# Kernel optimization log

Measured on AMD Instinct MI355X. Metric: run time of the kernel, lower is better.

Reference implementation:

```python
import jax, jax.numpy as jnp
import numpy as np

B, P, EPG = 1000, 100, 1200  # graphs, nodes/graph, edges/graph
IN, HID, OUT, K = 16, 64, 5, 3


def setup_inputs() -> dict:
    key = jax.random.key(0)
    ks = jax.random.split(key, 12)
    offs = jnp.repeat(jnp.arange(B, dtype=jnp.int32) * P, EPG)
    src = jax.random.randint(ks[0], (B * EPG,), 0, P, dtype=jnp.int32) + offs
    dst = jax.random.randint(ks[1], (B * EPG,), 0, P, dtype=jnp.int32) + offs
    graph_ids = jnp.repeat(jnp.arange(B, dtype=jnp.int32), P)
    feat = jax.random.normal(ks[2], (B * P, IN), dtype=jnp.float32)

    def lin(k1, fan_in, fan_out):
        s = 1.0 / np.sqrt(fan_in)
        return jax.random.uniform(k1, (fan_in, fan_out), jnp.float32, -s, s)

    return {
        'feat': feat, 'src': src, 'dst': dst, 'graph_ids': graph_ids,
        'n_graphs': B,
        'W1': lin(ks[3], K * IN, HID), 'b1': jnp.zeros((HID,), jnp.float32),
        'W2': lin(ks[4], K * HID, HID), 'b2': jnp.zeros((HID,), jnp.float32),
        'W3': lin(ks[5], K * HID, HID), 'b3': jnp.zeros((HID,), jnp.float32),
        'Wfc': lin(ks[6], HID, OUT), 'bfc': jnp.zeros((OUT,), jnp.float32),
    }


def _cheb_conv(x, src, dst, d_invsqrt, W, b, k):
    # DGL ChebConv with lambda_max=2 -> re_norm=1, scaled Laplacian = -D^-1/2 A D^-1/2
    n = x.shape[0]

    def Ax(h):
        msg = (h * d_invsqrt)[src]                      # gather from source nodes
        agg = jax.ops.segment_sum(msg, dst, num_segments=n)
        return agg * d_invsqrt

    Xs = [x]
    if k > 1:
        Xs.append(-Ax(Xs[0]))                           # X1 = L_hat X0
        for _ in range(2, k):
            Xs.append(-2.0 * Ax(Xs[-1]) - Xs[-2])       # X_i = 2 L_hat X_{i-1} - X_{i-2}
    Xt = jnp.concatenate(Xs, axis=1)                    # [n, k*f]
    return Xt @ W + b


def reference(feat, src, dst, graph_ids, n_graphs, W1, b1, W2, b2, W3, b3, Wfc, bfc):
    n = feat.shape[0]
    deg = jax.ops.segment_sum(jnp.ones((src.shape[0],), feat.dtype), dst, num_segments=n)
    d_invsqrt = jnp.where(deg < 1.0, 1.0, deg) ** -0.5
    d_invsqrt = d_invsqrt[:, None]

    h = jax.nn.relu(_cheb_conv(feat, src, dst, d_invsqrt, W1, b1, K))
    h = jax.nn.relu(_cheb_conv(h, src, dst, d_invsqrt, W2, b2, K))
    h = jax.nn.relu(_cheb_conv(h, src, dst, d_invsqrt, W3, b3, K))

    # dgl.mean_nodes: per-graph mean pooling
    counts = jax.ops.segment_sum(jnp.ones((n,), h.dtype), graph_ids, num_segments=n_graphs)
    hg = jax.ops.segment_sum(h, graph_ids, num_segments=n_graphs) / counts[:, None]
    return hg @ Wfc + bfc
```

## Files before the change

### kernel.cpp

```cpp
#include <hip/hip_runtime.h>

#define NGRAPH 1000
#define P      100
#define EPG    1200
#define INF    16
#define HID    64
#define NOUT   5


#define ASTR   100
#define T1OFF  64
#define T2OFF  80

#define AINT_K  128
#define AINT_SZ (P * AINT_K)

#define RK1 64
#define RK2 208
#define L1HI 0
#define L1LO 4096
#define L2HI 8192
#define L2LO 21504
#define L3HI 34816
#define L3LO 48128
#define WT_SHORTS 61440

typedef short short8 __attribute__((ext_vector_type(8)));
typedef float f32x4  __attribute__((ext_vector_type(4)));
typedef int   int4v  __attribute__((ext_vector_type(4)));

__device__ __forceinline__ int sw(int row, int col) {
    return row * ASTR + (col ^ (((row >> 3) & 3) << 3));
}

__device__ __forceinline__ unsigned packsplit(float x) {
    unsigned u  = __float_as_uint(x);
    unsigned hi = (u + 0x7fffu + ((u >> 16) & 1u)) >> 16;
    float r = x - __uint_as_float(hi << 16);
    unsigned v  = __float_as_uint(r);
    unsigned lo = (v + 0x7fffu + ((v >> 16) & 1u)) >> 16;
    return (hi << 16) | (lo & 0xffffu);
}

__device__ __forceinline__ float unpack(unsigned p) {
    return __uint_as_float(p & 0xffff0000u) + __uint_as_float(p << 16);
}

#define PSEL_HI 0x07060302u
#define PSEL_LO 0x05040100u

__global__ __launch_bounds__(256) void wprep(
    const float* __restrict__ W1, const float* __restrict__ W2,
    const float* __restrict__ W3, short* __restrict__ wt)
{
    const int i0 = blockIdx.x * blockDim.x + threadIdx.x;
    const int stride = gridDim.x * blockDim.x;
    for (int e = i0; e < HID * RK1; e += stride) {
        int c = e / RK1, r = e % RK1;
        float v = (r < 3 * INF) ? W1[r * HID + c] : 0.f;
        unsigned p = packsplit(v);
        wt[L1HI + e] = (short)(p >> 16);
        wt[L1LO + e] = (short)(p & 0xffffu);
    }
    for (int e = i0; e < HID * RK2; e += stride) {
        int c = e / RK2, r = e % RK2;
        float v2 = (r < 3 * HID) ? W2[r * HID + c] : 0.f;
        float v3 = (r < 3 * HID) ? W3[r * HID + c] : 0.f;
        unsigned p2 = packsplit(v2), p3 = packsplit(v3);
        wt[L2HI + e] = (short)(p2 >> 16); wt[L2LO + e] = (short)(p2 & 0xffffu);
        wt[L3HI + e] = (short)(p3 >> 16); wt[L3LO + e] = (short)(p3 & 0xffffu);
    }
}

__global__ __launch_bounds__(256) void abuild(
    const int* __restrict__ src, const int* __restrict__ dst,
    short* __restrict__ aint)
{
    __shared__ unsigned int cnt[AINT_SZ / 2];
    const int g = blockIdx.x, tid = threadIdx.x, base = g * P;
    for (int i = tid; i < AINT_SZ / 2; i += 256) cnt[i] = 0u;
    __syncthreads();
    const int* srcg = src + g * EPG;
    const int* dstg = dst + g * EPG;
    for (int e = tid; e < EPG; e += 256) {
        int s = srcg[e] - base;
        int d = dstg[e] - base;
        int idx = d * AINT_K + s;
        atomicAdd(&cnt[idx >> 1], 1u << ((idx & 1) * 16));
    }
    __syncthreads();
    unsigned int* outw = (unsigned int*)(aint + (size_t)g * AINT_SZ);
    for (int i = tid; i < AINT_SZ / 2; i += 256) {
        unsigned int u = cnt[i];
        unsigned int b0 = __float_as_uint((float)(u & 0xffffu)) >> 16;
        unsigned int b1 = __float_as_uint((float)(u >> 16)) >> 16;
        outw[i] = b0 | (b1 << 16);
    }
}

template <int SECOND>
__device__ __forceinline__ void dense_prop(
    unsigned* __restrict__ Ap,
    short8 a00, short8 a01, short8 a02, short8 a03,
    short8 a10, short8 a11, short8 a12, short8 a13,
    bool has2, int srcoff, int dstoff, int ycb,
    int rb0, int rb1, f32x4 dv0, f32x4 dv1, int lane)
{
    const int n16 = lane & 15;
    const int q   = lane >> 4;
    const int kq  = q * 8;
    const int c   = srcoff + n16;
    f32x4 p0, p1;
    p0[0]=0.f; p0[1]=0.f; p0[2]=0.f; p0[3]=0.f;
    p1[0]=0.f; p1[1]=0.f; p1[2]=0.f; p1[3]=0.f;

#define PROPK(KK, A0, A1) { \
    const int rr = KK * 32 + kq; \
    const unsigned u0 = Ap[sw((KK < 3 || rr + 0 < P) ? rr + 0 : 0, c)]; \
    const unsigned u1 = Ap[sw((KK < 3 || rr + 1 < P) ? rr + 1 : 0, c)]; \
    const unsigned u2 = Ap[sw((KK < 3 || rr + 2 < P) ? rr + 2 : 0, c)]; \
    const unsigned u3 = Ap[sw((KK < 3 || rr + 3 < P) ? rr + 3 : 0, c)]; \
    const unsigned u4 = Ap[sw((KK < 3 || rr + 4 < P) ? rr + 4 : 0, c)]; \
    const unsigned u5 = Ap[sw((KK < 3 || rr + 5 < P) ? rr + 5 : 0, c)]; \
    const unsigned u6 = Ap[sw((KK < 3 || rr + 6 < P) ? rr + 6 : 0, c)]; \
    const unsigned u7 = Ap[sw((KK < 3 || rr + 7 < P) ? rr + 7 : 0, c)]; \
    int4v hh, ll; \
    hh[0] = (int)__builtin_amdgcn_perm(u1, u0, PSEL_HI); \
    hh[1] = (int)__builtin_amdgcn_perm(u3, u2, PSEL_HI); \
    hh[2] = (int)__builtin_amdgcn_perm(u5, u4, PSEL_HI); \
    hh[3] = (int)__builtin_amdgcn_perm(u7, u6, PSEL_HI); \
    ll[0] = (int)__builtin_amdgcn_perm(u1, u0, PSEL_LO); \
    ll[1] = (int)__builtin_amdgcn_perm(u3, u2, PSEL_LO); \
    ll[2] = (int)__builtin_amdgcn_perm(u5, u4, PSEL_LO); \
    ll[3] = (int)__builtin_amdgcn_perm(u7, u6, PSEL_LO); \
    const short8 bhi = __builtin_bit_cast(short8, hh); \
    const short8 blo = __builtin_bit_cast(short8, ll); \
    p0 = __builtin_amdgcn_mfma_f32_16x16x32_bf16(A0, bhi, p0, 0, 0, 0); \
    p0 = __builtin_amdgcn_mfma_f32_16x16x32_bf16(A0, blo, p0, 0, 0, 0); \
    if (has2) { \
        p1 = __builtin_amdgcn_mfma_f32_16x16x32_bf16(A1, bhi, p1, 0, 0, 0); \
        p1 = __builtin_amdgcn_mfma_f32_16x16x32_bf16(A1, blo, p1, 0, 0, 0); \
    } }

    PROPK(0, a00, a10)
    PROPK(1, a01, a11)
    PROPK(2, a02, a12)
    PROPK(3, a03, a13)
#undef PROPK

#pragma unroll
    for (int r = 0; r < 4; r++) {
        const int row = rb0 + q * 4 + r;
        const float d2 = dv0[r] * dv0[r];
        float o;
        if (SECOND) o = -2.f * d2 * p0[r] - unpack(Ap[sw(row, ycb + n16)]);
        else        o = -d2 * p0[r];
        Ap[sw(row, dstoff + n16)] = packsplit(o);
    }
    if (has2) {
#pragma unroll
        for (int r = 0; r < 4; r++) {
            const int row = rb1 + q * 4 + r;
            if (rb1 != 84 || row >= 96) {
                const float d2 = dv1[r] * dv1[r];
                float o;
                if (SECOND) o = -2.f * d2 * p1[r] - unpack(Ap[sw(row, ycb + n16)]);
                else        o = -d2 * p1[r];
                Ap[sw(row, dstoff + n16)] = packsplit(o);
            }
        }
    }
}

template <int F, int FINAL>
__device__ __forceinline__ void cheb_layer(
    unsigned* __restrict__ Ap, const float* __restrict__ dinv,
    short8 a00, short8 a01, short8 a02, short8 a03,
    short8 a10, short8 a11, short8 a12, short8 a13, bool has2,
    const short* __restrict__ whi, const short* __restrict__ wlo,
    const float* __restrict__ bias,
    int tid, int rb0, int rb1, f32x4 dv0, f32x4 dv1)
{
    const int RK   = 3 * F + 16;
    const int lane = tid & 63;
    const int wv   = tid >> 6;
    const int n16  = lane & 15;
    const int q    = lane >> 4;
    const int ncol = (wv << 4) + n16;

    f32x4 acc[7];
#pragma unroll
    for (int t = 0; t < 7; t++) { acc[t][0]=0.f; acc[t][1]=0.f; acc[t][2]=0.f; acc[t][3]=0.f; }

    for (int cb = 0; cb < F; cb += 16) {
        dense_prop<0>(Ap, a00,a01,a02,a03, a10,a11,a12,a13, has2,
                      cb,    T1OFF, 0,  rb0, rb1, dv0, dv1, lane);
        __syncthreads();
        dense_prop<1>(Ap, a00,a01,a02,a03, a10,a11,a12,a13, has2,
                      T1OFF, T2OFF, cb, rb0, rb1, dv0, dv1, lane);
        __syncthreads();

#pragma unroll
        for (int ks = 0; ks < 2; ks++) {
            int wr, aoff;
            if (ks == 0) {
                wr   = (q == 0) ? cb : (q == 1) ? cb + 8 : (q == 2) ? F + cb : F + cb + 8;
                aoff = (q == 0) ? cb : (q == 1) ? cb + 8 : (q == 2) ? T1OFF  : T1OFF + 8;
            } else {
                wr   = (q == 0) ? 2*F + cb : (q == 1) ? 2*F + cb + 8 : (q == 2) ? 3*F : 3*F + 8;
                aoff = (q == 0) ? T2OFF    : (q == 1) ? T2OFF + 8    : (q == 2) ? T1OFF : T1OFF + 8;
            }
            const short8 bhi = *(const short8*)&whi[ncol * RK + wr];
            const short8 blo = *(const short8*)&wlo[ncol * RK + wr];
#pragma unroll
            for (int t = 0; t < 7; t++) {
                const int row = ((t < 6) ? t * 16 : 84) + n16;
                const unsigned* xp = &Ap[sw(row, aoff)];
                const int4v w0 = *(const int4v*)xp;
                const int4v w1 = *(const int4v*)(xp + 4);
                int4v hh, ll;
                hh[0] = (int)__builtin_amdgcn_perm((unsigned)w0[1], (unsigned)w0[0], PSEL_HI);
                hh[1] = (int)__builtin_amdgcn_perm((unsigned)w0[3], (unsigned)w0[2], PSEL_HI);
                hh[2] = (int)__builtin_amdgcn_perm((unsigned)w1[1], (unsigned)w1[0], PSEL_HI);
                hh[3] = (int)__builtin_amdgcn_perm((unsigned)w1[3], (unsigned)w1[2], PSEL_HI);
                ll[0] = (int)__builtin_amdgcn_perm((unsigned)w0[1], (unsigned)w0[0], PSEL_LO);
                ll[1] = (int)__builtin_amdgcn_perm((unsigned)w0[3], (unsigned)w0[2], PSEL_LO);
                ll[2] = (int)__builtin_amdgcn_perm((unsigned)w1[1], (unsigned)w1[0], PSEL_LO);
                ll[3] = (int)__builtin_amdgcn_perm((unsigned)w1[3], (unsigned)w1[2], PSEL_LO);
                const short8 ahi = __builtin_bit_cast(short8, hh);
                const short8 alo = __builtin_bit_cast(short8, ll);
                acc[t] = __builtin_amdgcn_mfma_f32_16x16x32_bf16(ahi, bhi, acc[t], 0, 0, 0);
                acc[t] = __builtin_amdgcn_mfma_f32_16x16x32_bf16(ahi, blo, acc[t], 0, 0, 0);
                acc[t] = __builtin_amdgcn_mfma_f32_16x16x32_bf16(alo, bhi, acc[t], 0, 0, 0);
            }
        }
        __syncthreads();
    }

    const float bcol = bias[ncol];
#pragma unroll
    for (int t = 0; t < 7; t++) {
        const int rbase = ((t < 6) ? t * 16 : 84) + q * 4;
#pragma unroll
        for (int r = 0; r < 4; r++) {
            const int row = rbase + r;
            if (t < 6 || row >= 96) {
                const float dn = dinv[row];
                const float v = acc[t][r];
                float o;
                if (FINAL) o = fmaxf(v * (1.0f / dn) + bcol, 0.f);
                else       o = fmaxf(v + bcol * dn, 0.f);
                Ap[sw(row, ncol)] = packsplit(o);
            }
        }
    }
    __syncthreads();
}

__global__ __launch_bounds__(256, 4) void gnn_kernel(
    const float* __restrict__ feat,
    const int* __restrict__ src, const int* __restrict__ dst,
    const float* __restrict__ b1, const float* __restrict__ b2,
    const float* __restrict__ b3,
    const float* __restrict__ Wfc, const float* __restrict__ bfc,
    const short* __restrict__ wt, const short* __restrict__ aint,
    float* __restrict__ out)
{
    __shared__ __align__(16) unsigned Ap[P * ASTR];
    __shared__ float meta[128];

    const int g = blockIdx.x;
    const int tid = threadIdx.x;
    const int base = g * P;
    const int* dstg = dst + g * EPG;

    int* deg = (int*)meta;
    for (int i = tid; i < P; i += 256) deg[i] = 0;
    __syncthreads();
    for (int e = tid; e < EPG; e += 256) atomicAdd(&deg[dstg[e] - base], 1);
    __syncthreads();
    for (int i = tid; i < P; i += 256) {
        int dg = deg[i];
        meta[i] = rsqrtf((float)(dg > 1 ? dg : 1));
    }
    __syncthreads();

    for (int i = tid; i < P * INF / 4; i += 256) {
        int n = i >> 2, f0 = (i & 3) * 4;
        float4 v = *(const float4*)&feat[(size_t)base * INF + i * 4];
        float dn = meta[n];
        int4v pk;
        pk[0] = (int)packsplit(v.x * dn);
        pk[1] = (int)packsplit(v.y * dn);
        pk[2] = (int)packsplit(v.z * dn);
        pk[3] = (int)packsplit(v.w * dn);
        *(int4v*)&Ap[sw(n, f0)] = pk;
    }
    __syncthreads();

    const int lane = tid & 63, wv = tid >> 6, q = lane >> 4, n16 = lane & 15;
    const int rb0 = wv * 16;
    const int t2i = wv + 4;
    const int rb1 = (t2i >= 6) ? 84 : t2i * 16;
    const bool has2 = (wv < 3);
    f32x4 dv0, dv1;
#pragma unroll
    for (int r = 0; r < 4; r++) {
        dv0[r] = meta[rb0 + q * 4 + r];
        dv1[r] = meta[(has2 ? rb1 : rb0) + q * 4 + r];
    }
    const short* aintg = aint + (size_t)g * AINT_SZ;
    const int arow0 = rb0 + n16;
    const int arow1 = (has2 ? rb1 : rb0) + n16;
    const short8 a00 = *(const short8*)&aintg[arow0 * AINT_K +  0 + q * 8];
    const short8 a01 = *(const short8*)&aintg[arow0 * AINT_K + 32 + q * 8];
    const short8 a02 = *(const short8*)&aintg[arow0 * AINT_K + 64 + q * 8];
    const short8 a03 = *(const short8*)&aintg[arow0 * AINT_K + 96 + q * 8];
    const short8 a10 = *(const short8*)&aintg[arow1 * AINT_K +  0 + q * 8];
    const short8 a11 = *(const short8*)&aintg[arow1 * AINT_K + 32 + q * 8];
    const short8 a12 = *(const short8*)&aintg[arow1 * AINT_K + 64 + q * 8];
    const short8 a13 = *(const short8*)&aintg[arow1 * AINT_K + 96 + q * 8];

    cheb_layer<INF, 0>(Ap, meta, a00,a01,a02,a03, a10,a11,a12,a13, has2,
                       wt + L1HI, wt + L1LO, b1, tid, rb0, rb1, dv0, dv1);
    cheb_layer<HID, 0>(Ap, meta, a00,a01,a02,a03, a10,a11,a12,a13, has2,
                       wt + L2HI, wt + L2LO, b2, tid, rb0, rb1, dv0, dv1);
    cheb_layer<HID, 1>(Ap, meta, a00,a01,a02,a03, a10,a11,a12,a13, has2,
                       wt + L3HI, wt + L3LO, b3, tid, rb0, rb1, dv0, dv1);

    {
        const int l = tid & 63, w = tid >> 6;
        float s = 0.f;
        for (int n = w; n < P; n += 4) s += unpack(Ap[sw(n, l)]);
        float o0 = s * Wfc[l * NOUT + 0];
        float o1 = s * Wfc[l * NOUT + 1];
        float o2 = s * Wfc[l * NOUT + 2];
        float o3 = s * Wfc[l * NOUT + 3];
        float o4 = s * Wfc[l * NOUT + 4];
#pragma unroll
        for (int d = 1; d < 64; d <<= 1) {
            o0 += __shfl_xor(o0, d);
            o1 += __shfl_xor(o1, d);
            o2 += __shfl_xor(o2, d);
            o3 += __shfl_xor(o3, d);
            o4 += __shfl_xor(o4, d);
        }
        if (l == 0) {
            meta[100 + w * NOUT + 0] = o0;
            meta[100 + w * NOUT + 1] = o1;
            meta[100 + w * NOUT + 2] = o2;
            meta[100 + w * NOUT + 3] = o3;
            meta[100 + w * NOUT + 4] = o4;
        }
    }
    __syncthreads();
    if (tid < NOUT) {
        float o = meta[100 + tid] + meta[105 + tid] + meta[110 + tid] + meta[115 + tid];
        out[g * NOUT + tid] = bfc[tid] + o * (1.0f / P);
    }
}

extern "C" void kernel_launch(void* const* d_in, const int* in_sizes, int n_in,
                              void* d_out, int out_size, void* d_ws, size_t ws_size,
                              hipStream_t stream)
{
    const float* feat = (const float*)d_in[0];
    const int*   src  = (const int*)d_in[1];
    const int*   dst  = (const int*)d_in[2];
    const float* W1  = (const float*)d_in[5];
    const float* b1  = (const float*)d_in[6];
    const float* W2  = (const float*)d_in[7];
    const float* b2  = (const float*)d_in[8];
    const float* W3  = (const float*)d_in[9];
    const float* b3  = (const float*)d_in[10];
    const float* Wfc = (const float*)d_in[11];
    const float* bfc = (const float*)d_in[12];
    float* out = (float*)d_out;

    short* wt   = (short*)d_ws;
    short* aint = wt + WT_SHORTS;

    wprep<<<64, 256, 0, stream>>>(W1, W2, W3, wt);
    abuild<<<NGRAPH, 256, 0, stream>>>(src, dst, aint);
    gnn_kernel<<<NGRAPH, 256, 0, stream>>>(feat, src, dst,
                                           b1, b2, b3, Wfc, bfc, wt, aint, out);
}
```

Before: 180.8 us.

## Fuse adjacency build into main kernel and split feature LDS into hi/lo planes

```diff
diff --git a/kernel.cpp b/kernel.cpp
--- a/kernel.cpp
+++ b/kernel.cpp
@@ -8,12 +8,9 @@
 #define NOUT   5
 
 
-#define ASTR   100
+#define FSTR   96
 #define T1OFF  64
 #define T2OFF  80
-
-#define AINT_K  128
-#define AINT_SZ (P * AINT_K)
 
 #define RK1 64
 #define RK2 208
@@ -23,14 +20,12 @@
 #define L2LO 21504
 #define L3HI 34816
 #define L3LO 48128
-#define WT_SHORTS 61440
 
 typedef short short8 __attribute__((ext_vector_type(8)));
 typedef float f32x4  __attribute__((ext_vector_type(4)));
-typedef int   int4v  __attribute__((ext_vector_type(4)));
-
-__device__ __forceinline__ int sw(int row, int col) {
-    return row * ASTR + (col ^ (((row >> 3) & 3) << 3));
+
+__device__ __forceinline__ int swf(int row, int col) {
+    return row * FSTR + (col ^ (((row >> 3) & 3) << 3));
 }
 
 __device__ __forceinline__ unsigned packsplit(float x) {
@@ -42,12 +37,10 @@
     return (hi << 16) | (lo & 0xffffu);
 }
 
-__device__ __forceinline__ float unpack(unsigned p) {
-    return __uint_as_float(p & 0xffff0000u) + __uint_as_float(p << 16);
-}
-
-#define PSEL_HI 0x07060302u
-#define PSEL_LO 0x05040100u
+__device__ __forceinline__ float up2(short h, short l) {
+    return __uint_as_float(((unsigned)(unsigned short)h) << 16) +
+           __uint_as_float(((unsigned)(unsigned short)l) << 16);
+}
 
 __global__ __launch_bounds__(256) void wprep(
     const float* __restrict__ W1, const float* __restrict__ W2,
@@ -72,35 +65,9 @@
     }
 }
 
-__global__ __launch_bounds__(256) void abuild(
-    const int* __restrict__ src, const int* __restrict__ dst,
-    short* __restrict__ aint)
-{
-    __shared__ unsigned int cnt[AINT_SZ / 2];
-    const int g = blockIdx.x, tid = threadIdx.x, base = g * P;
-    for (int i = tid; i < AINT_SZ / 2; i += 256) cnt[i] = 0u;
-    __syncthreads();
-    const int* srcg = src + g * EPG;
-    const int* dstg = dst + g * EPG;
-    for (int e = tid; e < EPG; e += 256) {
-        int s = srcg[e] - base;
-        int d = dstg[e] - base;
-        int idx = d * AINT_K + s;
-        atomicAdd(&cnt[idx >> 1], 1u << ((idx & 1) * 16));
-    }
-    __syncthreads();
-    unsigned int* outw = (unsigned int*)(aint + (size_t)g * AINT_SZ);
-    for (int i = tid; i < AINT_SZ / 2; i += 256) {
-        unsigned int u = cnt[i];
-        unsigned int b0 = __float_as_uint((float)(u & 0xffffu)) >> 16;
-        unsigned int b1 = __float_as_uint((float)(u >> 16)) >> 16;
-        outw[i] = b0 | (b1 << 16);
-    }
-}
-
 template <int SECOND>
 __device__ __forceinline__ void dense_prop(
-    unsigned* __restrict__ Ap,
+    short* __restrict__ Ahi, short* __restrict__ Alo,
     short8 a00, short8 a01, short8 a02, short8 a03,
     short8 a10, short8 a11, short8 a12, short8 a13,
     bool has2, int srcoff, int dstoff, int ycb,
@@ -109,32 +76,38 @@
     const int n16 = lane & 15;
     const int q   = lane >> 4;
     const int kq  = q * 8;
-    const int c   = srcoff + n16;
+    const int c = (srcoff + n16) ^ (q << 3);
     f32x4 p0, p1;
     p0[0]=0.f; p0[1]=0.f; p0[2]=0.f; p0[3]=0.f;
     p1[0]=0.f; p1[1]=0.f; p1[2]=0.f; p1[3]=0.f;
 
 #define PROPK(KK, A0, A1) { \
-    const int rr = KK * 32 + kq; \
-    const unsigned u0 = Ap[sw((KK < 3 || rr + 0 < P) ? rr + 0 : 0, c)]; \
-    const unsigned u1 = Ap[sw((KK < 3 || rr + 1 < P) ? rr + 1 : 0, c)]; \
-    const unsigned u2 = Ap[sw((KK < 3 || rr + 2 < P) ? rr + 2 : 0, c)]; \
-    const unsigned u3 = Ap[sw((KK < 3 || rr + 3 < P) ? rr + 3 : 0, c)]; \
-    const unsigned u4 = Ap[sw((KK < 3 || rr + 4 < P) ? rr + 4 : 0, c)]; \
-    const unsigned u5 = Ap[sw((KK < 3 || rr + 5 < P) ? rr + 5 : 0, c)]; \
-    const unsigned u6 = Ap[sw((KK < 3 || rr + 6 < P) ? rr + 6 : 0, c)]; \
-    const unsigned u7 = Ap[sw((KK < 3 || rr + 7 < P) ? rr + 7 : 0, c)]; \
-    int4v hh, ll; \
-    hh[0] = (int)__builtin_amdgcn_perm(u1, u0, PSEL_HI); \
-    hh[1] = (int)__builtin_amdgcn_perm(u3, u2, PSEL_HI); \
-    hh[2] = (int)__builtin_amdgcn_perm(u5, u4, PSEL_HI); \
-    hh[3] = (int)__builtin_amdgcn_perm(u7, u6, PSEL_HI); \
-    ll[0] = (int)__builtin_amdgcn_perm(u1, u0, PSEL_LO); \
-    ll[1] = (int)__builtin_amdgcn_perm(u3, u2, PSEL_LO); \
-    ll[2] = (int)__builtin_amdgcn_perm(u5, u4, PSEL_LO); \
-    ll[3] = (int)__builtin_amdgcn_perm(u7, u6, PSEL_LO); \
-    const short8 bhi = __builtin_bit_cast(short8, hh); \
-    const short8 blo = __builtin_bit_cast(short8, ll); \
+    const int b0 = (KK * 32 + kq) * FSTR + c; \
+    short8 bhi, blo; \
+    if (KK < 3) { \
+        bhi[0]=Ahi[b0        ]; blo[0]=Alo[b0        ]; \
+        bhi[1]=Ahi[b0+1*FSTR ]; blo[1]=Alo[b0+1*FSTR ]; \
+        bhi[2]=Ahi[b0+2*FSTR ]; blo[2]=Alo[b0+2*FSTR ]; \
+        bhi[3]=Ahi[b0+3*FSTR ]; blo[3]=Alo[b0+3*FSTR ]; \
+        bhi[4]=Ahi[b0+4*FSTR ]; blo[4]=Alo[b0+4*FSTR ]; \
+        bhi[5]=Ahi[b0+5*FSTR ]; blo[5]=Alo[b0+5*FSTR ]; \
+        bhi[6]=Ahi[b0+6*FSTR ]; blo[6]=Alo[b0+6*FSTR ]; \
+        bhi[7]=Ahi[b0+7*FSTR ]; blo[7]=Alo[b0+7*FSTR ]; \
+    } else { \
+        const int m0 = 96 + kq; \
+        const int i0 = (m0+0 < P ? (m0+0)*FSTR : 0) + c; \
+        const int i1 = (m0+1 < P ? (m0+1)*FSTR : 0) + c; \
+        const int i2 = (m0+2 < P ? (m0+2)*FSTR : 0) + c; \
+        const int i3 = (m0+3 < P ? (m0+3)*FSTR : 0) + c; \
+        bhi[0]=Ahi[i0]; blo[0]=Alo[i0]; \
+        bhi[1]=Ahi[i1]; blo[1]=Alo[i1]; \
+        bhi[2]=Ahi[i2]; blo[2]=Alo[i2]; \
+        bhi[3]=Ahi[i3]; blo[3]=Alo[i3]; \
+        bhi[4]=0; blo[4]=0; \
+        bhi[5]=0; blo[5]=0; \
+        bhi[6]=0; blo[6]=0; \
+        bhi[7]=0; blo[7]=0; \
+    } \
     p0 = __builtin_amdgcn_mfma_f32_16x16x32_bf16(A0, bhi, p0, 0, 0, 0); \
     p0 = __builtin_amdgcn_mfma_f32_16x16x32_bf16(A0, blo, p0, 0, 0, 0); \
     if (has2) { \
@@ -153,9 +126,13 @@
         const int row = rb0 + q * 4 + r;
         const float d2 = dv0[r] * dv0[r];
         float o;
-        if (SECOND) o = -2.f * d2 * p0[r] - unpack(Ap[sw(row, ycb + n16)]);
-        else        o = -d2 * p0[r];
-        Ap[sw(row, dstoff + n16)] = packsplit(o);
+        if (SECOND) {
+            const int yi = swf(row, ycb + n16);
+            o = -2.f * d2 * p0[r] - up2(Ahi[yi], Alo[yi]);
+        } else o = -d2 * p0[r];
+        const int di = swf(row, dstoff + n16);
+        const unsigned pp = packsplit(o);
+        Ahi[di] = (short)(pp >> 16); Alo[di] = (short)pp;
     }
     if (has2) {
 #pragma unroll
@@ -164,9 +141,13 @@
             if (rb1 != 84 || row >= 96) {
                 const float d2 = dv1[r] * dv1[r];
                 float o;
-                if (SECOND) o = -2.f * d2 * p1[r] - unpack(Ap[sw(row, ycb + n16)]);
-                else        o = -d2 * p1[r];
-                Ap[sw(row, dstoff + n16)] = packsplit(o);
+                if (SECOND) {
+                    const int yi = swf(row, ycb + n16);
+                    o = -2.f * d2 * p1[r] - up2(Ahi[yi], Alo[yi]);
+                } else o = -d2 * p1[r];
+                const int di = swf(row, dstoff + n16);
+                const unsigned pp = packsplit(o);
+                Ahi[di] = (short)(pp >> 16); Alo[di] = (short)pp;
             }
         }
     }
@@ -174,7 +155,8 @@
 
 template <int F, int FINAL>
 __device__ __forceinline__ void cheb_layer(
-    unsigned* __restrict__ Ap, const float* __restrict__ dinv,
+    short* __restrict__ Ahi, short* __restrict__ Alo,
+    const float* __restrict__ dinv,
     short8 a00, short8 a01, short8 a02, short8 a03,
     short8 a10, short8 a11, short8 a12, short8 a13, bool has2,
     const short* __restrict__ whi, const short* __restrict__ wlo,
@@ -193,10 +175,10 @@
     for (int t = 0; t < 7; t++) { acc[t][0]=0.f; acc[t][1]=0.f; acc[t][2]=0.f; acc[t][3]=0.f; }
 
     for (int cb = 0; cb < F; cb += 16) {
-        dense_prop<0>(Ap, a00,a01,a02,a03, a10,a11,a12,a13, has2,
+        dense_prop<0>(Ahi, Alo, a00,a01,a02,a03, a10,a11,a12,a13, has2,
                       cb,    T1OFF, 0,  rb0, rb1, dv0, dv1, lane);
         __syncthreads();
-        dense_prop<1>(Ap, a00,a01,a02,a03, a10,a11,a12,a13, has2,
+        dense_prop<1>(Ahi, Alo, a00,a01,a02,a03, a10,a11,a12,a13, has2,
                       T1OFF, T2OFF, cb, rb0, rb1, dv0, dv1, lane);
         __syncthreads();
 
@@ -215,20 +197,9 @@
 #pragma unroll
             for (int t = 0; t < 7; t++) {
                 const int row = ((t < 6) ? t * 16 : 84) + n16;
-                const unsigned* xp = &Ap[sw(row, aoff)];
-                const int4v w0 = *(const int4v*)xp;
-                const int4v w1 = *(const int4v*)(xp + 4);
-                int4v hh, ll;
-                hh[0] = (int)__builtin_amdgcn_perm((unsigned)w0[1], (unsigned)w0[0], PSEL_HI);
-                hh[1] = (int)__builtin_amdgcn_perm((unsigned)w0[3], (unsigned)w0[2], PSEL_HI);
-                hh[2] = (int)__builtin_amdgcn_perm((unsigned)w1[1], (unsigned)w1[0], PSEL_HI);
-                hh[3] = (int)__builtin_amdgcn_perm((unsigned)w1[3], (unsigned)w1[2], PSEL_HI);
-                ll[0] = (int)__builtin_amdgcn_perm((unsigned)w0[1], (unsigned)w0[0], PSEL_LO);
-                ll[1] = (int)__builtin_amdgcn_perm((unsigned)w0[3], (unsigned)w0[2], PSEL_LO);
-                ll[2] = (int)__builtin_amdgcn_perm((unsigned)w1[1], (unsigned)w1[0], PSEL_LO);
-                ll[3] = (int)__builtin_amdgcn_perm((unsigned)w1[3], (unsigned)w1[2], PSEL_LO);
-                const short8 ahi = __builtin_bit_cast(short8, hh);
-                const short8 alo = __builtin_bit_cast(short8, ll);
+                const int ax  = row * FSTR + (aoff ^ (((row >> 3) & 3) << 3));
+                const short8 ahi = *(const short8*)&Ahi[ax];
+                const short8 alo = *(const short8*)&Alo[ax];
                 acc[t] = __builtin_amdgcn_mfma_f32_16x16x32_bf16(ahi, bhi, acc[t], 0, 0, 0);
                 acc[t] = __builtin_amdgcn_mfma_f32_16x16x32_bf16(ahi, blo, acc[t], 0, 0, 0);
                 acc[t] = __builtin_amdgcn_mfma_f32_16x16x32_bf16(alo, bhi, acc[t], 0, 0, 0);
@@ -250,7 +221,9 @@
                 float o;
                 if (FINAL) o = fmaxf(v * (1.0f / dn) + bcol, 0.f);
                 else       o = fmaxf(v + bcol * dn, 0.f);
-                Ap[sw(row, ncol)] = packsplit(o);
+                const int oi = swf(row, ncol);
+                const unsigned pp = packsplit(o);
+                Ahi[oi] = (short)(pp >> 16); Alo[oi] = (short)pp;
             }
         }
     }
@@ -263,75 +236,98 @@
     const float* __restrict__ b1, const float* __restrict__ b2,
     const float* __restrict__ b3,
     const float* __restrict__ Wfc, const float* __restrict__ bfc,
-    const short* __restrict__ wt, const short* __restrict__ aint,
+    const short* __restrict__ wt,
     float* __restrict__ out)
 {
-    __shared__ __align__(16) unsigned Ap[P * ASTR];
+    __shared__ __align__(16) unsigned ldsu[9728];
     __shared__ float meta[128];
+    short* Ahi = (short*)ldsu;
+    short* Alo = (short*)ldsu + 9600;
+    unsigned* cnt = ldsu;
 
     const int g = blockIdx.x;
     const int tid = threadIdx.x;
     const int base = g * P;
+    const int* srcg = src + g * EPG;
     const int* dstg = dst + g * EPG;
 
     int* deg = (int*)meta;
+    for (int i = tid; i < 6400; i += 256) cnt[i] = 0u;
     for (int i = tid; i < P; i += 256) deg[i] = 0;
     __syncthreads();
-    for (int e = tid; e < EPG; e += 256) atomicAdd(&deg[dstg[e] - base], 1);
+    for (int e = tid; e < EPG; e += 256) {
+        int s = srcg[e] - base;
+        int d = dstg[e] - base;
+        atomicAdd(&deg[d], 1);
+        atomicAdd(&cnt[d * 64 + (s >> 1)], 1u << ((s & 1) * 16));
+    }
     __syncthreads();
     for (int i = tid; i < P; i += 256) {
         int dg = deg[i];
         meta[i] = rsqrtf((float)(dg > 1 ? dg : 1));
     }
-    __syncthreads();
-
-    for (int i = tid; i < P * INF / 4; i += 256) {
-        int n = i >> 2, f0 = (i & 3) * 4;
-        float4 v = *(const float4*)&feat[(size_t)base * INF + i * 4];
-        float dn = meta[n];
-        int4v pk;
-        pk[0] = (int)packsplit(v.x * dn);
-        pk[1] = (int)packsplit(v.y * dn);
-        pk[2] = (int)packsplit(v.z * dn);
-        pk[3] = (int)packsplit(v.w * dn);
-        *(int4v*)&Ap[sw(n, f0)] = pk;
-    }
-    __syncthreads();
-
     const int lane = tid & 63, wv = tid >> 6, q = lane >> 4, n16 = lane & 15;
     const int rb0 = wv * 16;
     const int t2i = wv + 4;
     const int rb1 = (t2i >= 6) ? 84 : t2i * 16;
     const bool has2 = (wv < 3);
+    const int arow0 = rb0 + n16;
+    const int arow1 = (has2 ? rb1 : rb0) + n16;
+    short8 a00, a01, a02, a03, a10, a11, a12, a13;
+#define MKA(VAR, AR, KK) { \
+    const unsigned w0 = cnt[(AR) * 64 + (KK) * 16 + q * 4 + 0]; \
+    const unsigned w1 = cnt[(AR) * 64 + (KK) * 16 + q * 4 + 1]; \
+    const unsigned w2 = cnt[(AR) * 64 + (KK) * 16 + q * 4 + 2]; \
+    const unsigned w3 = cnt[(AR) * 64 + (KK) * 16 + q * 4 + 3]; \
+    short8 t; \
+    t[0] = (short)(__float_as_uint((float)(w0 & 0xffffu)) >> 16); \
+    t[1] = (short)(__float_as_uint((float)(w0 >> 16))     >> 16); \
+    t[2] = (short)(__float_as_uint((float)(w1 & 0xffffu)) >> 16); \
+    t[3] = (short)(__float_as_uint((float)(w1 >> 16))     >> 16); \
+    t[4] = (short)(__float_as_uint((float)(w2 & 0xffffu)) >> 16); \
+    t[5] = (short)(__float_as_uint((float)(w2 >> 16))     >> 16); \
+    t[6] = (short)(__float_as_uint((float)(w3 & 0xffffu)) >> 16); \
+    t[7] = (short)(__float_as_uint((float)(w3 >> 16))     >> 16); \
+    VAR = t; }
+    MKA(a00, arow0, 0)  MKA(a01, arow0, 1)  MKA(a02, arow0, 2)  MKA(a03, arow0, 3)
+    MKA(a10, arow1, 0)  MKA(a11, arow1, 1)  MKA(a12, arow1, 2)  MKA(a13, arow1, 3)
+#undef MKA
+    __syncthreads();
+
     f32x4 dv0, dv1;
 #pragma unroll
     for (int r = 0; r < 4; r++) {
         dv0[r] = meta[rb0 + q * 4 + r];
         dv1[r] = meta[(has2 ? rb1 : rb0) + q * 4 + r];
     }
-    const short* aintg = aint + (size_t)g * AINT_SZ;
-    const int arow0 = rb0 + n16;
-    const int arow1 = (has2 ? rb1 : rb0) + n16;
-    const short8 a00 = *(const short8*)&aintg[arow0 * AINT_K +  0 + q * 8];
-    const short8 a01 = *(const short8*)&aintg[arow0 * AINT_K + 32 + q * 8];
-    const short8 a02 = *(const short8*)&aintg[arow0 * AINT_K + 64 + q * 8];
-    const short8 a03 = *(const short8*)&aintg[arow0 * AINT_K + 96 + q * 8];
-    const short8 a10 = *(const short8*)&aintg[arow1 * AINT_K +  0 + q * 8];
-    const short8 a11 = *(const short8*)&aintg[arow1 * AINT_K + 32 + q * 8];
-    const short8 a12 = *(const short8*)&aintg[arow1 * AINT_K + 64 + q * 8];
-    const short8 a13 = *(const short8*)&aintg[arow1 * AINT_K + 96 + q * 8];
-
-    cheb_layer<INF, 0>(Ap, meta, a00,a01,a02,a03, a10,a11,a12,a13, has2,
+    for (int i = tid; i < P * INF / 4; i += 256) {
+        int n = i >> 2, f0 = (i & 3) * 4;
+        float4 v = *(const float4*)&feat[(size_t)base * INF + i * 4];
+        float dn = meta[n];
+        unsigned p0 = packsplit(v.x * dn), p1 = packsplit(v.y * dn);
+        unsigned p2 = packsplit(v.z * dn), p3 = packsplit(v.w * dn);
+        const int bi = swf(n, f0);
+        *(unsigned*)&Ahi[bi]     = (p0 >> 16) | (p1 & 0xffff0000u);
+        *(unsigned*)&Ahi[bi + 2] = (p2 >> 16) | (p3 & 0xffff0000u);
+        *(unsigned*)&Alo[bi]     = (p0 & 0xffffu) | (p1 << 16);
+        *(unsigned*)&Alo[bi + 2] = (p2 & 0xffffu) | (p3 << 16);
+    }
+    __syncthreads();
+
+    cheb_layer<INF, 0>(Ahi, Alo, meta, a00,a01,a02,a03, a10,a11,a12,a13, has2,
                        wt + L1HI, wt + L1LO, b1, tid, rb0, rb1, dv0, dv1);
-    cheb_layer<HID, 0>(Ap, meta, a00,a01,a02,a03, a10,a11,a12,a13, has2,
+    cheb_layer<HID, 0>(Ahi, Alo, meta, a00,a01,a02,a03, a10,a11,a12,a13, has2,
                        wt + L2HI, wt + L2LO, b2, tid, rb0, rb1, dv0, dv1);
-    cheb_layer<HID, 1>(Ap, meta, a00,a01,a02,a03, a10,a11,a12,a13, has2,
+    cheb_layer<HID, 1>(Ahi, Alo, meta, a00,a01,a02,a03, a10,a11,a12,a13, has2,
                        wt + L3HI, wt + L3LO, b3, tid, rb0, rb1, dv0, dv1);
 
     {
         const int l = tid & 63, w = tid >> 6;
         float s = 0.f;
-        for (int n = w; n < P; n += 4) s += unpack(Ap[sw(n, l)]);
+        for (int n = w; n < P; n += 4) {
+            const int ii = swf(n, l);
+            s += up2(Ahi[ii], Alo[ii]);
+        }
         float o0 = s * Wfc[l * NOUT + 0];
         float o1 = s * Wfc[l * NOUT + 1];
         float o2 = s * Wfc[l * NOUT + 2];
@@ -377,11 +373,9 @@
     const float* bfc = (const float*)d_in[12];
     float* out = (float*)d_out;
 
-    short* wt   = (short*)d_ws;
-    short* aint = wt + WT_SHORTS;
+    short* wt = (short*)d_ws;
 
     wprep<<<64, 256, 0, stream>>>(W1, W2, W3, wt);
-    abuild<<<NGRAPH, 256, 0, stream>>>(src, dst, aint);
     gnn_kernel<<<NGRAPH, 256, 0, stream>>>(feat, src, dst,
-                                           b1, b2, b3, Wfc, bfc, wt, aint, out);
-}
+                                           b1, b2, b3, Wfc, bfc, wt, out);
+}
```

Result: slower. 193.1 us (+6.8%).

## Reload adjacency fragments from global per use and tighten LDS stride with new swizzle

Applied to the files above, without the earlier changes.

```diff
diff --git a/kernel.cpp b/kernel.cpp
--- a/kernel.cpp
+++ b/kernel.cpp
@@ -8,7 +8,7 @@
 #define NOUT   5
 
 
-#define ASTR   100
+#define ASTR   96
 #define T1OFF  64
 #define T2OFF  80
 
@@ -29,8 +29,9 @@
 typedef float f32x4  __attribute__((ext_vector_type(4)));
 typedef int   int4v  __attribute__((ext_vector_type(4)));
 
-__device__ __forceinline__ int sw(int row, int col) {
-    return row * ASTR + (col ^ (((row >> 3) & 3) << 3));
+__device__ __forceinline__ int swf(int row, int col) {
+    return row * ASTR +
+           (col ^ ((((row >> 3) & 1) << 4) | (((row >> 1) & 3) << 2)));
 }
 
 __device__ __forceinline__ unsigned packsplit(float x) {
@@ -100,30 +101,31 @@
 
 template <int SECOND>
 __device__ __forceinline__ void dense_prop(
-    unsigned* __restrict__ Ap,
-    short8 a00, short8 a01, short8 a02, short8 a03,
-    short8 a10, short8 a11, short8 a12, short8 a13,
-    bool has2, int srcoff, int dstoff, int ycb,
+    unsigned* __restrict__ Ap, const short* __restrict__ aintg,
+    int arow0, int arow1, bool has2,
+    int srcoff, int dstoff, int ycb,
     int rb0, int rb1, f32x4 dv0, f32x4 dv1, int lane)
 {
     const int n16 = lane & 15;
     const int q   = lane >> 4;
     const int kq  = q * 8;
-    const int c   = srcoff + n16;
+    const int cc  = srcoff + n16;
     f32x4 p0, p1;
     p0[0]=0.f; p0[1]=0.f; p0[2]=0.f; p0[3]=0.f;
     p1[0]=0.f; p1[1]=0.f; p1[2]=0.f; p1[3]=0.f;
 
-#define PROPK(KK, A0, A1) { \
-    const int rr = KK * 32 + kq; \
-    const unsigned u0 = Ap[sw((KK < 3 || rr + 0 < P) ? rr + 0 : 0, c)]; \
-    const unsigned u1 = Ap[sw((KK < 3 || rr + 1 < P) ? rr + 1 : 0, c)]; \
-    const unsigned u2 = Ap[sw((KK < 3 || rr + 2 < P) ? rr + 2 : 0, c)]; \
-    const unsigned u3 = Ap[sw((KK < 3 || rr + 3 < P) ? rr + 3 : 0, c)]; \
-    const unsigned u4 = Ap[sw((KK < 3 || rr + 4 < P) ? rr + 4 : 0, c)]; \
-    const unsigned u5 = Ap[sw((KK < 3 || rr + 5 < P) ? rr + 5 : 0, c)]; \
-    const unsigned u6 = Ap[sw((KK < 3 || rr + 6 < P) ? rr + 6 : 0, c)]; \
-    const unsigned u7 = Ap[sw((KK < 3 || rr + 7 < P) ? rr + 7 : 0, c)]; \
+#define PROPK(KK) { \
+    const short8 a0 = *(const short8*)&aintg[arow0 * AINT_K + KK * 32 + kq]; \
+    const short8 a1 = *(const short8*)&aintg[arow1 * AINT_K + KK * 32 + kq]; \
+    const int r0 = KK * 32 + kq; \
+    const unsigned u0 = Ap[swf((KK < 3 || r0 + 0 < P) ? r0 + 0 : 0, cc)]; \
+    const unsigned u1 = Ap[swf((KK < 3 || r0 + 1 < P) ? r0 + 1 : 0, cc)]; \
+    const unsigned u2 = Ap[swf((KK < 3 || r0 + 2 < P) ? r0 + 2 : 0, cc)]; \
+    const unsigned u3 = Ap[swf((KK < 3 || r0 + 3 < P) ? r0 + 3 : 0, cc)]; \
+    const unsigned u4 = Ap[swf((KK < 3 || r0 + 4 < P) ? r0 + 4 : 0, cc)]; \
+    const unsigned u5 = Ap[swf((KK < 3 || r0 + 5 < P) ? r0 + 5 : 0, cc)]; \
+    const unsigned u6 = Ap[swf((KK < 3 || r0 + 6 < P) ? r0 + 6 : 0, cc)]; \
+    const unsigned u7 = Ap[swf((KK < 3 || r0 + 7 < P) ? r0 + 7 : 0, cc)]; \
     int4v hh, ll; \
     hh[0] = (int)__builtin_amdgcn_perm(u1, u0, PSEL_HI); \
     hh[1] = (int)__builtin_amdgcn_perm(u3, u2, PSEL_HI); \
@@ -135,17 +137,17 @@
     ll[3] = (int)__builtin_amdgcn_perm(u7, u6, PSEL_LO); \
     const short8 bhi = __builtin_bit_cast(short8, hh); \
     const short8 blo = __builtin_bit_cast(short8, ll); \
-    p0 = __builtin_amdgcn_mfma_f32_16x16x32_bf16(A0, bhi, p0, 0, 0, 0); \
-    p0 = __builtin_amdgcn_mfma_f32_16x16x32_bf16(A0, blo, p0, 0, 0, 0); \
+    p0 = __builtin_amdgcn_mfma_f32_16x16x32_bf16(a0, bhi, p0, 0, 0, 0); \
+    p0 = __builtin_amdgcn_mfma_f32_16x16x32_bf16(a0, blo, p0, 0, 0, 0); \
     if (has2) { \
-        p1 = __builtin_amdgcn_mfma_f32_16x16x32_bf16(A1, bhi, p1, 0, 0, 0); \
-        p1 = __builtin_amdgcn_mfma_f32_16x16x32_bf16(A1, blo, p1, 0, 0, 0); \
+        p1 = __builtin_amdgcn_mfma_f32_16x16x32_bf16(a1, bhi, p1, 0, 0, 0); \
+        p1 = __builtin_amdgcn_mfma_f32_16x16x32_bf16(a1, blo, p1, 0, 0, 0); \
     } }
 
-    PROPK(0, a00, a10)
-    PROPK(1, a01, a11)
-    PROPK(2, a02, a12)
-    PROPK(3, a03, a13)
+    PROPK(0)
+    PROPK(1)
+    PROPK(2)
+    PROPK(3)
 #undef PROPK
 
 #pragma unroll
@@ -153,9 +155,9 @@
         const int row = rb0 + q * 4 + r;
         const float d2 = dv0[r] * dv0[r];
         float o;
-        if (SECOND) o = -2.f * d2 * p0[r] - unpack(Ap[sw(row, ycb + n16)]);
+        if (SECOND) o = -2.f * d2 * p0[r] - unpack(Ap[swf(row, ycb + n16)]);
         else        o = -d2 * p0[r];
-        Ap[sw(row, dstoff + n16)] = packsplit(o);
+        Ap[swf(row, dstoff + n16)] = packsplit(o);
     }
     if (has2) {
 #pragma unroll
@@ -164,9 +166,9 @@
             if (rb1 != 84 || row >= 96) {
                 const float d2 = dv1[r] * dv1[r];
                 float o;
-                if (SECOND) o = -2.f * d2 * p1[r] - unpack(Ap[sw(row, ycb + n16)]);
+                if (SECOND) o = -2.f * d2 * p1[r] - unpack(Ap[swf(row, ycb + n16)]);
                 else        o = -d2 * p1[r];
-                Ap[sw(row, dstoff + n16)] = packsplit(o);
+                Ap[swf(row, dstoff + n16)] = packsplit(o);
             }
         }
     }
@@ -175,8 +177,7 @@
 template <int F, int FINAL>
 __device__ __forceinline__ void cheb_layer(
     unsigned* __restrict__ Ap, const float* __restrict__ dinv,
-    short8 a00, short8 a01, short8 a02, short8 a03,
-    short8 a10, short8 a11, short8 a12, short8 a13, bool has2,
+    const short* __restrict__ aintg, int arow0, int arow1, bool has2,
     const short* __restrict__ whi, const short* __restrict__ wlo,
     const float* __restrict__ bias,
     int tid, int rb0, int rb1, f32x4 dv0, f32x4 dv1)
@@ -193,10 +194,10 @@
     for (int t = 0; t < 7; t++) { acc[t][0]=0.f; acc[t][1]=0.f; acc[t][2]=0.f; acc[t][3]=0.f; }
 
     for (int cb = 0; cb < F; cb += 16) {
-        dense_prop<0>(Ap, a00,a01,a02,a03, a10,a11,a12,a13, has2,
+        dense_prop<0>(Ap, aintg, arow0, arow1, has2,
                       cb,    T1OFF, 0,  rb0, rb1, dv0, dv1, lane);
         __syncthreads();
-        dense_prop<1>(Ap, a00,a01,a02,a03, a10,a11,a12,a13, has2,
+        dense_prop<1>(Ap, aintg, arow0, arow1, has2,
                       T1OFF, T2OFF, cb, rb0, rb1, dv0, dv1, lane);
         __syncthreads();
 
@@ -215,9 +216,8 @@
 #pragma unroll
             for (int t = 0; t < 7; t++) {
                 const int row = ((t < 6) ? t * 16 : 84) + n16;
-                const unsigned* xp = &Ap[sw(row, aoff)];
-                const int4v w0 = *(const int4v*)xp;
-                const int4v w1 = *(const int4v*)(xp + 4);
+                const int4v w0 = *(const int4v*)&Ap[swf(row, aoff)];
+                const int4v w1 = *(const int4v*)&Ap[swf(row, aoff + 4)];
                 int4v hh, ll;
                 hh[0] = (int)__builtin_amdgcn_perm((unsigned)w0[1], (unsigned)w0[0], PSEL_HI);
                 hh[1] = (int)__builtin_amdgcn_perm((unsigned)w0[3], (unsigned)w0[2], PSEL_HI);
@@ -250,7 +250,7 @@
                 float o;
                 if (FINAL) o = fmaxf(v * (1.0f / dn) + bcol, 0.f);
                 else       o = fmaxf(v + bcol * dn, 0.f);
-                Ap[sw(row, ncol)] = packsplit(o);
+                Ap[swf(row, ncol)] = packsplit(o);
             }
         }
     }
@@ -294,7 +294,7 @@
         pk[1] = (int)packsplit(v.y * dn);
         pk[2] = (int)packsplit(v.z * dn);
         pk[3] = (int)packsplit(v.w * dn);
-        *(int4v*)&Ap[sw(n, f0)] = pk;
+        *(int4v*)&Ap[swf(n, f0)] = pk;
     }
     __syncthreads();
 
@@ -312,26 +312,18 @@
     const short* aintg = aint + (size_t)g * AINT_SZ;
     const int arow0 = rb0 + n16;
     const int arow1 = (has2 ? rb1 : rb0) + n16;
-    const short8 a00 = *(const short8*)&aintg[arow0 * AINT_K +  0 + q * 8];
-    const short8 a01 = *(const short8*)&aintg[arow0 * AINT_K + 32 + q * 8];
-    const short8 a02 = *(const short8*)&aintg[arow0 * AINT_K + 64 + q * 8];
-    const short8 a03 = *(const short8*)&aintg[arow0 * AINT_K + 96 + q * 8];
-    const short8 a10 = *(const short8*)&aintg[arow1 * AINT_K +  0 + q * 8];
-    const short8 a11 = *(const short8*)&aintg[arow1 * AINT_K + 32 + q * 8];
-    const short8 a12 = *(const short8*)&aintg[arow1 * AINT_K + 64 + q * 8];
-    const short8 a13 = *(const short8*)&aintg[arow1 * AINT_K + 96 + q * 8];
-
-    cheb_layer<INF, 0>(Ap, meta, a00,a01,a02,a03, a10,a11,a12,a13, has2,
+
+    cheb_layer<INF, 0>(Ap, meta, aintg, arow0, arow1, has2,
                        wt + L1HI, wt + L1LO, b1, tid, rb0, rb1, dv0, dv1);
-    cheb_layer<HID, 0>(Ap, meta, a00,a01,a02,a03, a10,a11,a12,a13, has2,
+    cheb_layer<HID, 0>(Ap, meta, aintg, arow0, arow1, has2,
                        wt + L2HI, wt + L2LO, b2, tid, rb0, rb1, dv0, dv1);
-    cheb_layer<HID, 1>(Ap, meta, a00,a01,a02,a03, a10,a11,a12,a13, has2,
+    cheb_layer<HID, 1>(Ap, meta, aintg, arow0, arow1, has2,
                        wt + L3HI, wt + L3LO, b3, tid, rb0, rb1, dv0, dv1);
 
     {
         const int l = tid & 63, w = tid >> 6;
         float s = 0.f;
-        for (int n = w; n < P; n += 4) s += unpack(Ap[sw(n, l)]);
+        for (int n = w; n < P; n += 4) s += unpack(Ap[swf(n, l)]);
         float o0 = s * Wfc[l * NOUT + 0];
         float o1 = s * Wfc[l * NOUT + 1];
         float o2 = s * Wfc[l * NOUT + 2];
```

Result: slower. 258.6 us (+43.0%).
